# Kernel tuning notes

Hardware: AMD Instinct MI355X
Metric: run time of the kernel (lower is better)

## Reference

```python
import jax, jax.numpy as jnp
import numpy as np

N, E, B = 40000, 640000, 8192
IN, META, HID, OUT = 768, 6, 256, 128
NE, K, REL, NET = 4, 2, 200, 3
NL, NH, FF = 4, 4, 512


def setup_inputs():
    key = jax.random.key(0)
    keys = iter(jax.random.split(key, 64))
    def p(*shape):
        return jax.random.normal(next(keys), shape, jnp.float32) * 0.02
    return dict(
        x=jax.random.normal(next(keys), (N, IN + META), jnp.float32),
        noise=jax.random.normal(next(keys), (3, B, NE), jnp.float32),
        g_lin1_w=p(HID, IN + META), g_lin1_b=p(HID),
        conv_W=p(2, HID, HID), conv_Wr=p(2, HID, REL), conv_a=p(2, 3 * HID),
        conv_Wres=p(2, HID, HID), conv_rel=p(2, NET, REL),
        g_lin2_w=p(OUT, HID), g_lin2_b=p(OUT),
        te_w=p(OUT, IN), te_b=p(OUT),
        me_w1=p(HID, META), me_b1=p(HID), me_w2=p(OUT, HID), me_b2=p(OUT),
        moe_gate_w=p(3, NE, OUT), moe_noise_w=p(3, OUT),
        moe_w1=p(3, NE, 4 * OUT, OUT), moe_b1=p(3, NE, 4 * OUT),
        moe_w2=p(3, NE, OUT, 4 * OUT), moe_b2=p(3, NE, OUT),
        tf_qkv_w=p(NL, 3 * OUT, OUT), tf_qkv_b=p(NL, 3 * OUT),
        tf_out_w=p(NL, OUT, OUT), tf_out_b=p(NL, OUT),
        tf_ln1_g=jnp.ones((NL, OUT), jnp.float32), tf_ln1_b=jnp.zeros((NL, OUT), jnp.float32),
        tf_ff1_w=p(NL, FF, OUT), tf_ff1_b=p(NL, FF),
        tf_ff2_w=p(NL, OUT, FF), tf_ff2_b=p(NL, OUT),
        tf_ln2_g=jnp.ones((NL, OUT), jnp.float32), tf_ln2_b=jnp.zeros((NL, OUT), jnp.float32),
        clf_w=p(2, 3 * OUT), clf_b=p(2),
        edge_index=jax.random.randint(next(keys), (2, E), 0, N),
        edge_type=jax.random.randint(next(keys), (E,), 0, NET),
        batch_size=B,
    )


def _seg_softmax(logit, seg, n):
    m = jax.ops.segment_max(logit, seg, num_segments=n)
    e = jnp.exp(logit - m[seg])
    s = jax.ops.segment_sum(e, seg, num_segments=n)
    return e / (s[seg] + 1e-16)


def _hgn_layer(h, src, dst, et, W, Wr, a, Wres, rel, final):
    n, d = h.shape[0], W.shape[0]
    Wx = h @ W.T  # [N, HID]
    # a(cat(Wx_i, Wx_j, Wr_rel)) decomposed: per-node + per-edge-type scalars
    s_i = Wx @ a[:d]
    s_j = Wx @ a[d:2 * d]
    r_s = (rel @ Wr.T) @ a[2 * d:]  # [NET]
    logit = jax.nn.leaky_relu(s_i[dst] + s_j[src] + r_s[et], 0.2)
    alpha = _seg_softmax(logit, dst, n)
    agg = jax.ops.segment_sum(Wx[src] * alpha[:, None], dst, num_segments=n)
    out = jax.nn.elu(agg + h @ Wres.T)
    if final:
        out = out / jnp.maximum(jnp.linalg.norm(out, axis=1, keepdims=True), 1e-12)
    return out


def _moe(xv, eps, gate_w, noise_w, w1, b1, w2, b2):
    g = xv @ gate_w.T                       # [B, NE]
    nsd = jax.nn.softplus(xv @ noise_w)     # [B]
    h = g + eps * nsd[:, None]
    _, bot = jax.lax.top_k(-h, K)           # bottom-K experts get -inf
    drop = jnp.sum(jax.nn.one_hot(bot, NE, dtype=h.dtype), axis=1) > 0
    h = jnp.where(drop, -jnp.inf, h)
    L = jax.nn.softmax(h, axis=1)
    logits, idx = jax.lax.top_k(L, K)
    tmp = L.sum(0)
    loss = (jnp.std(tmp, ddof=1) / jnp.mean(tmp)) ** 2
    comb = jnp.einsum('bs,bse->be', logits, jax.nn.one_hot(idx, NE, dtype=L.dtype))
    h1 = jax.nn.relu(jnp.einsum('bd,ehd->ebh', xv, w1) + b1[:, None, :])
    eo = jnp.einsum('ebh,eoh->ebo', h1, w2) + b2[:, None, :]  # [NE, B, OUT]
    return jnp.einsum('be,ebo->bo', comb, eo), loss


def _ln(x, g, b):
    mu = x.mean(-1, keepdims=True)
    var = x.var(-1, keepdims=True)
    return (x - mu) / jnp.sqrt(var + 1e-5) * g + b


def _tf_layer(x, qkv_w, qkv_b, out_w, out_b, ln1g, ln1b, f1w, f1b, f2w, f2b, ln2g, ln2b):
    Bq, S, D = x.shape
    hd = D // NH
    qkv = x @ qkv_w.T + qkv_b
    q, k, v = jnp.split(qkv, 3, axis=-1)
    q = q.reshape(Bq, S, NH, hd)
    k = k.reshape(Bq, S, NH, hd)
    v = v.reshape(Bq, S, NH, hd)
    att = jax.nn.softmax(jnp.einsum('bshd,bthd->bhst', q, k) / jnp.sqrt(jnp.float32(hd)), axis=-1)
    o = jnp.einsum('bhst,bthd->bshd', att, v).reshape(Bq, S, D)
    x = _ln(x + o @ out_w.T + out_b, ln1g, ln1b)
    ff = jax.nn.relu(x @ f1w.T + f1b) @ f2w.T + f2b
    return _ln(x + ff, ln2g, ln2b)


def _forward(x, noise, g_lin1_w, g_lin1_b, conv_W, conv_Wr, conv_a, conv_Wres, conv_rel,
             g_lin2_w, g_lin2_b, te_w, te_b, me_w1, me_b1, me_w2, me_b2,
             moe_gate_w, moe_noise_w, moe_w1, moe_b1, moe_w2, moe_b2,
             tf_qkv_w, tf_qkv_b, tf_out_w, tf_out_b, tf_ln1_g, tf_ln1_b,
             tf_ff1_w, tf_ff1_b, tf_ff2_w, tf_ff2_b, tf_ln2_g, tf_ln2_b,
             clf_w, clf_b, edge_index, edge_type, batch_size):
    src, dst = edge_index[0], edge_index[1]
    # graph encoder (dropout is eval no-op)
    h = jax.nn.relu(x @ g_lin1_w.T + g_lin1_b)
    h = _hgn_layer(h, src, dst, edge_type, conv_W[0], conv_Wr[0], conv_a[0], conv_Wres[0], conv_rel[0], False)
    h = _hgn_layer(h, src, dst, edge_type, conv_W[1], conv_Wr[1], conv_a[1], conv_Wres[1], conv_rel[1], True)
    graph = jax.nn.relu(h @ g_lin2_w.T + g_lin2_b)
    x_g = graph[:batch_size]
    text = x[:batch_size, :IN]
    meta = x[:batch_size, IN:]
    x_t = jax.nn.relu(text @ te_w.T + te_b)
    x_m = jax.nn.relu(jax.nn.relu(meta @ me_w1.T + me_b1) @ me_w2.T + me_b2)
    outs, losses = [], []
    for i, xv in enumerate((x_g, x_t, x_m)):
        o, l = _moe(xv, noise[i], moe_gate_w[i], moe_noise_w[i], moe_w1[i], moe_b1[i], moe_w2[i], moe_b2[i])
        outs.append(o)
        losses.append(l)
    loss = losses[0] + losses[1] + losses[2]
    z = jnp.stack(outs, axis=1)  # [B, 3, OUT]
    for li in range(NL):
        z = _tf_layer(z, tf_qkv_w[li], tf_qkv_b[li], tf_out_w[li], tf_out_b[li],
                      tf_ln1_g[li], tf_ln1_b[li], tf_ff1_w[li], tf_ff1_b[li],
                      tf_ff2_w[li], tf_ff2_b[li], tf_ln2_g[li], tf_ln2_b[li])
    logits = z.reshape(z.shape[0], -1) @ clf_w.T + clf_b
    return logits, loss


def reference(x, noise, g_lin1_w, g_lin1_b, conv_W, conv_Wr, conv_a, conv_Wres, conv_rel,
              g_lin2_w, g_lin2_b, te_w, te_b, me_w1, me_b1, me_w2, me_b2,
              moe_gate_w, moe_noise_w, moe_w1, moe_b1, moe_w2, moe_b2,
              tf_qkv_w, tf_qkv_b, tf_out_w, tf_out_b, tf_ln1_g, tf_ln1_b,
              tf_ff1_w, tf_ff1_b, tf_ff2_w, tf_ff2_b, tf_ln2_g, tf_ln2_b,
              clf_w, clf_b, edge_index, edge_type, batch_size):
    return _forward(x, noise, g_lin1_w, g_lin1_b, conv_W, conv_Wr, conv_a, conv_Wres, conv_rel,
                    g_lin2_w, g_lin2_b, te_w, te_b, me_w1, me_b1, me_w2, me_b2,
                    moe_gate_w, moe_noise_w, moe_w1, moe_b1, moe_w2, moe_b2,
                    tf_qkv_w, tf_qkv_b, tf_out_w, tf_out_b, tf_ln1_g, tf_ln1_b,
                    tf_ff1_w, tf_ff1_b, tf_ff2_w, tf_ff2_b, tf_ln2_g, tf_ln2_b,
                    clf_w, clf_b, edge_index, edge_type, batch_size)
```

## Files before the change

### kernel.cpp

```cpp
#include <hip/hip_runtime.h>
#include <hip/hip_bf16.h>
#include <math.h>

#define NN 40000
#define EE 640000
#define BB 8192
#define IN_DIM 768
#define META_DIM 6
#define XDIM 774
#define HID 256
#define OUT_D 128
#define NEXP 4
#define NET_T 3
#define REL_D 200
#define NLAY 4
#define FF_D 512

typedef __attribute__((ext_vector_type(8))) short short8;
typedef __attribute__((ext_vector_type(4))) float f32x4;

__device__ __forceinline__ ushort f2bf(float f) {
    union { float f; unsigned u; } a; a.f = f;
    unsigned u = a.u;
    unsigned r = (u + 0x7FFFu + ((u >> 16) & 1u)) >> 16;
    return (ushort)r;
}
__device__ __forceinline__ float bf2f(ushort h) {
    union { unsigned u; float f; } a; a.u = ((unsigned)h) << 16;
    return a.f;
}
__device__ __forceinline__ unsigned packsplit(float v) {
    ushort h = f2bf(v);
    ushort lo = f2bf(v - bf2f(h));
    return ((unsigned)h << 16) | lo;
}

__global__ void cvt_pack_kernel(const float* __restrict__ src, int ldsrc, int Kreal,
                                unsigned* __restrict__ pk, int R, int ldp)
{
    size_t i = (size_t)blockIdx.x * blockDim.x + threadIdx.x;
    size_t total = (size_t)R * ldp;
    if (i >= total) return;
    int col = (int)(i % ldp);
    int row = (int)(i / ldp);
    float v = (col < Kreal) ? src[(size_t)row * ldsrc + col] : 0.f;
    pk[i] = packsplit(v);
}

static void cvt_pack(const float* src, int ldsrc, int Kreal, unsigned* pk,
                     int R, int ldp, hipStream_t s)
{
    size_t total = (size_t)R * ldp;
    cvt_pack_kernel<<<(int)((total + 255) / 256), 256, 0, s>>>(src, ldsrc, Kreal, pk, R, ldp);
}

template<int ACT, int HAS_RES, int OUT_SPLIT, int A_FP32, int B_PACKED>
__global__ __launch_bounds__(256) void mfma3_128(
    const void* __restrict__ Ap, int lda, int Kreal,
    const void* __restrict__ Bp, int ldb,
    const float* __restrict__ bias, const float* __restrict__ res,
    float* __restrict__ C, unsigned* __restrict__ Cpk,
    int M, int Nn, int K)
{
    __shared__ __align__(16) ushort Ash[128 * 40];
    __shared__ __align__(16) ushort Asl[128 * 40];
    __shared__ __align__(16) ushort Bsh[128 * 40];
    __shared__ __align__(16) ushort Bsl[128 * 40];

    const unsigned* Ak = (const unsigned*)Ap;
    const float*    Af = (const float*)Ap;
    const unsigned* Bk = (const unsigned*)Bp;
    const float*    Bf = (const float*)Bp;

    int bn = blockIdx.x * 128;
    int bm = blockIdx.y * 128;
    int t = threadIdx.x;
    int wave = t >> 6, lane = t & 63;
    int wm = wave & 1, wn = wave >> 1;
    int quad = lane >> 4, r = lane & 15;

    uint4 apk[2][2];
    float afp[2][8];
    uint4 bpk[2][2];
    float bfp[2][8];

    auto loadA = [&](int k0) {
#pragma unroll
        for (int i = 0; i < 2; i++) {
            int idx = t + i * 256;
            int row = idx >> 2, c8 = idx & 3;
            int grow = bm + row; if (grow > M - 1) grow = M - 1;
            if (A_FP32) {
                int cb = k0 + c8 * 8;
                const float* p = Af + (size_t)grow * lda + cb;
                if (cb + 8 <= Kreal) {
                    float2 f0 = *(const float2*)p,       f1 = *(const float2*)(p + 2);
                    float2 f2 = *(const float2*)(p + 4), f3 = *(const float2*)(p + 6);
                    afp[i][0] = f0.x; afp[i][1] = f0.y; afp[i][2] = f1.x; afp[i][3] = f1.y;
                    afp[i][4] = f2.x; afp[i][5] = f2.y; afp[i][6] = f3.x; afp[i][7] = f3.y;
                } else {
#pragma unroll
                    for (int e = 0; e < 8; e++)
                        afp[i][e] = (cb + e < Kreal) ? p[e] : 0.f;
                }
            } else {
                const unsigned* p = Ak + (size_t)grow * lda + k0 + c8 * 8;
                apk[i][0] = *(const uint4*)p; apk[i][1] = *(const uint4*)(p + 4);
            }
        }
    };
    auto loadB = [&](int k0) {
#pragma unroll
        for (int i = 0; i < 2; i++) {
            int idx = t + i * 256;
            int row = idx >> 2, c8 = idx & 3;
            if (B_PACKED) {
                const unsigned* p = Bk + (size_t)(bn + row) * ldb + k0 + c8 * 8;
                bpk[i][0] = *(const uint4*)p; bpk[i][1] = *(const uint4*)(p + 4);
            } else {
                const float* p = Bf + (size_t)(bn + row) * ldb + k0 + c8 * 8;
                float2 f0 = *(const float2*)p,       f1 = *(const float2*)(p + 2);
                float2 f2 = *(const float2*)(p + 4), f3 = *(const float2*)(p + 6);
                bfp[i][0] = f0.x; bfp[i][1] = f0.y; bfp[i][2] = f1.x; bfp[i][3] = f1.y;
                bfp[i][4] = f2.x; bfp[i][5] = f2.y; bfp[i][6] = f3.x; bfp[i][7] = f3.y;
            }
        }
    };
    auto storeTiles = [&]() {
#pragma unroll
        for (int i = 0; i < 2; i++) {
            int idx = t + i * 256;
            int row = idx >> 2, c8 = idx & 3;
            short8 hi, lo;
            if (A_FP32) {
#pragma unroll
                for (int e = 0; e < 8; e++) {
                    ushort h = f2bf(afp[i][e]);
                    hi[e] = (short)h;
                    lo[e] = (short)f2bf(afp[i][e] - bf2f(h));
                }
            } else {
                unsigned u[8] = {apk[i][0].x, apk[i][0].y, apk[i][0].z, apk[i][0].w,
                                 apk[i][1].x, apk[i][1].y, apk[i][1].z, apk[i][1].w};
#pragma unroll
                for (int e = 0; e < 8; e++) { hi[e] = (short)(u[e] >> 16); lo[e] = (short)(u[e] & 0xFFFFu); }
            }
            *(short8*)&Ash[row * 40 + c8 * 8] = hi;
            *(short8*)&Asl[row * 40 + c8 * 8] = lo;
        }
#pragma unroll
        for (int i = 0; i < 2; i++) {
            int idx = t + i * 256;
            int row = idx >> 2, c8 = idx & 3;
            short8 hi, lo;
            if (B_PACKED) {
                unsigned u[8] = {bpk[i][0].x, bpk[i][0].y, bpk[i][0].z, bpk[i][0].w,
                                 bpk[i][1].x, bpk[i][1].y, bpk[i][1].z, bpk[i][1].w};
#pragma unroll
                for (int e = 0; e < 8; e++) { hi[e] = (short)(u[e] >> 16); lo[e] = (short)(u[e] & 0xFFFFu); }
            } else {
#pragma unroll
                for (int e = 0; e < 8; e++) {
                    ushort h = f2bf(bfp[i][e]);
                    hi[e] = (short)h;
                    lo[e] = (short)f2bf(bfp[i][e] - bf2f(h));
                }
            }
            *(short8*)&Bsh[row * 40 + c8 * 8] = hi;
            *(short8*)&Bsl[row * 40 + c8 * 8] = lo;
        }
    };

    f32x4 acc[4][4];
#pragma unroll
    for (int i = 0; i < 4; i++)
#pragma unroll
        for (int j = 0; j < 4; j++) acc[i][j] = (f32x4){0.f, 0.f, 0.f, 0.f};

    loadA(0); loadB(0);
    for (int k0 = 0; k0 < K; k0 += 32) {
        storeTiles();
        __syncthreads();
        if (k0 + 32 < K) { loadA(k0 + 32); loadB(k0 + 32); }

        short8 ah[4], al[4];
#pragma unroll
        for (int i = 0; i < 4; i++) {
            int ro = (wm * 64 + i * 16 + r) * 40 + quad * 8;
            ah[i] = *(const short8*)&Ash[ro];
            al[i] = *(const short8*)&Asl[ro];
        }
#pragma unroll
        for (int j = 0; j < 4; j++) {
            int ro = (wn * 64 + j * 16 + r) * 40 + quad * 8;
            short8 bh = *(const short8*)&Bsh[ro];
            short8 bl = *(const short8*)&Bsl[ro];
#pragma unroll
            for (int i = 0; i < 4; i++)
                acc[i][j] = __builtin_amdgcn_mfma_f32_16x16x32_bf16(ah[i], bh, acc[i][j], 0, 0, 0);
#pragma unroll
            for (int i = 0; i < 4; i++)
                acc[i][j] = __builtin_amdgcn_mfma_f32_16x16x32_bf16(ah[i], bl, acc[i][j], 0, 0, 0);
#pragma unroll
            for (int i = 0; i < 4; i++)
                acc[i][j] = __builtin_amdgcn_mfma_f32_16x16x32_bf16(al[i], bh, acc[i][j], 0, 0, 0);
        }
        __syncthreads();
    }

#pragma unroll
    for (int j = 0; j < 4; j++) {
        int col = bn + wn * 64 + j * 16 + r;
        float bc = bias ? bias[col] : 0.f;
#pragma unroll
        for (int i = 0; i < 4; i++) {
#pragma unroll
            for (int reg = 0; reg < 4; reg++) {
                int row = bm + wm * 64 + i * 16 + quad * 4 + reg;
                if (row >= M) continue;
                float v = acc[i][j][reg] + bc;
                if (HAS_RES) v += res[(size_t)row * Nn + col];
                if (ACT == 1) v = fmaxf(v, 0.f);
                else if (ACT == 2) v = (v > 0.f) ? v : expm1f(v);
                if (OUT_SPLIT) Cpk[(size_t)row * Nn + col] = packsplit(v);
                else           C[(size_t)row * Nn + col] = v;
            }
        }
    }
}

template<int ACT, int HAS_RES, int OUT_SPLIT, int A_FP32, int B_PACKED>
static void m128_launch(const void* Ap, int lda, int Kreal, const void* Bp, int ldb,
                        const float* bias, const float* res,
                        float* C, unsigned* Cpk,
                        int M, int Nn, int K, hipStream_t s)
{
    dim3 grid(Nn / 128, (M + 127) / 128);
    mfma3_128<ACT, HAS_RES, OUT_SPLIT, A_FP32, B_PACKED><<<grid, 256, 0, s>>>(
        Ap, lda, Kreal, Bp, ldb, bias, res, C, Cpk, M, Nn, K);
}

template<int WM, int ACT, int HAS_RES, int OUT_SPLIT, int A_FP32, int B_PACKED>
__global__ __launch_bounds__(256) void mfma3k(
    const void* __restrict__ Ap, int lda, int Kreal,
    const void* __restrict__ Bp, int ldb,
    const float* __restrict__ bias, const float* __restrict__ res,
    float* __restrict__ C, unsigned* __restrict__ Cpk,
    int M, int Nn, int K)
{
    const int BM = 32 * WM;
    __shared__ __align__(16) ushort Ash[BM * 40];
    __shared__ __align__(16) ushort Asl[BM * 40];
    __shared__ __align__(16) ushort Bsh[64 * 40];
    __shared__ __align__(16) ushort Bsl[64 * 40];

    const unsigned* Ak = (const unsigned*)Ap;
    const float*    Af = (const float*)Ap;
    const unsigned* Bk = (const unsigned*)Bp;
    const float*    Bf = (const float*)Bp;

    int bn = blockIdx.x * 64;
    int bm = blockIdx.y * BM;
    int t = threadIdx.x;
    int wave = t >> 6, lane = t & 63;
    int wm = wave & 1, wn = wave >> 1;
    int quad = lane >> 4, r = lane & 15;

    const int ACH = (BM * 4) / 256;

    uint4 apk[2][2];
    float afp[2][8];
    uint4 bpk[2];
    float4 bfp[2];

    auto loadA = [&](int k0) {
#pragma unroll
        for (int i = 0; i < ACH; i++) {
            int idx = t + i * 256;
            int row = idx >> 2, c8 = idx & 3;
            int grow = bm + row; if (grow > M - 1) grow = M - 1;
            if (A_FP32) {
                int cb = k0 + c8 * 8;
                const float* p = Af + (size_t)grow * lda + cb;
                if (cb + 8 <= Kreal) {
                    float2 f0 = *(const float2*)p,       f1 = *(const float2*)(p + 2);
                    float2 f2 = *(const float2*)(p + 4), f3 = *(const float2*)(p + 6);
                    afp[i][0] = f0.x; afp[i][1] = f0.y; afp[i][2] = f1.x; afp[i][3] = f1.y;
                    afp[i][4] = f2.x; afp[i][5] = f2.y; afp[i][6] = f3.x; afp[i][7] = f3.y;
                } else {
#pragma unroll
                    for (int e = 0; e < 8; e++)
                        afp[i][e] = (cb + e < Kreal) ? p[e] : 0.f;
                }
            } else {
                const unsigned* p = Ak + (size_t)grow * lda + k0 + c8 * 8;
                apk[i][0] = *(const uint4*)p; apk[i][1] = *(const uint4*)(p + 4);
            }
        }
    };
    auto loadB = [&](int k0) {
        int row = t >> 2, c8 = t & 3;
        if (B_PACKED) {
            const unsigned* p = Bk + (size_t)(bn + row) * ldb + k0 + c8 * 8;
            bpk[0] = *(const uint4*)p; bpk[1] = *(const uint4*)(p + 4);
        } else {
            const float* p = Bf + (size_t)(bn + row) * ldb + k0 + c8 * 8;
            bfp[0] = *(const float4*)p; bfp[1] = *(const float4*)(p + 4);
        }
    };
    auto storeTiles = [&]() {
#pragma unroll
        for (int i = 0; i < ACH; i++) {
            int idx = t + i * 256;
            int row = idx >> 2, c8 = idx & 3;
            short8 hi, lo;
            if (A_FP32) {
#pragma unroll
                for (int e = 0; e < 8; e++) {
                    ushort h = f2bf(afp[i][e]);
                    hi[e] = (short)h;
                    lo[e] = (short)f2bf(afp[i][e] - bf2f(h));
                }
            } else {
                unsigned u[8] = {apk[i][0].x, apk[i][0].y, apk[i][0].z, apk[i][0].w,
                                 apk[i][1].x, apk[i][1].y, apk[i][1].z, apk[i][1].w};
#pragma unroll
                for (int e = 0; e < 8; e++) { hi[e] = (short)(u[e] >> 16); lo[e] = (short)(u[e] & 0xFFFFu); }
            }
            *(short8*)&Ash[row * 40 + c8 * 8] = hi;
            *(short8*)&Asl[row * 40 + c8 * 8] = lo;
        }
        {
            int row = t >> 2, c8 = t & 3;
            short8 hi, lo;
            if (B_PACKED) {
                unsigned u[8] = {bpk[0].x, bpk[0].y, bpk[0].z, bpk[0].w,
                                 bpk[1].x, bpk[1].y, bpk[1].z, bpk[1].w};
#pragma unroll
                for (int e = 0; e < 8; e++) { hi[e] = (short)(u[e] >> 16); lo[e] = (short)(u[e] & 0xFFFFu); }
            } else {
                float f[8] = {bfp[0].x, bfp[0].y, bfp[0].z, bfp[0].w,
                              bfp[1].x, bfp[1].y, bfp[1].z, bfp[1].w};
#pragma unroll
                for (int e = 0; e < 8; e++) {
                    ushort h = f2bf(f[e]);
                    hi[e] = (short)h;
                    lo[e] = (short)f2bf(f[e] - bf2f(h));
                }
            }
            *(short8*)&Bsh[row * 40 + c8 * 8] = hi;
            *(short8*)&Bsl[row * 40 + c8 * 8] = lo;
        }
    };

    f32x4 acc[WM][2];
#pragma unroll
    for (int i = 0; i < WM; i++)
#pragma unroll
        for (int j = 0; j < 2; j++) acc[i][j] = (f32x4){0.f, 0.f, 0.f, 0.f};

    loadA(0); loadB(0);
    for (int k0 = 0; k0 < K; k0 += 32) {
        storeTiles();
        __syncthreads();
        if (k0 + 32 < K) { loadA(k0 + 32); loadB(k0 + 32); }

        short8 ah[WM], al[WM];
#pragma unroll
        for (int i = 0; i < WM; i++) {
            int ro = (wm * (WM * 16) + i * 16 + r) * 40 + quad * 8;
            ah[i] = *(const short8*)&Ash[ro];
            al[i] = *(const short8*)&Asl[ro];
        }
#pragma unroll
        for (int j = 0; j < 2; j++) {
            int ro = (wn * 32 + j * 16 + r) * 40 + quad * 8;
            short8 bh = *(const short8*)&Bsh[ro];
            short8 bl = *(const short8*)&Bsl[ro];
#pragma unroll
            for (int i = 0; i < WM; i++)
                acc[i][j] = __builtin_amdgcn_mfma_f32_16x16x32_bf16(ah[i], bh, acc[i][j], 0, 0, 0);
#pragma unroll
            for (int i = 0; i < WM; i++)
                acc[i][j] = __builtin_amdgcn_mfma_f32_16x16x32_bf16(ah[i], bl, acc[i][j], 0, 0, 0);
#pragma unroll
            for (int i = 0; i < WM; i++)
                acc[i][j] = __builtin_amdgcn_mfma_f32_16x16x32_bf16(al[i], bh, acc[i][j], 0, 0, 0);
        }
        __syncthreads();
    }

#pragma unroll
    for (int j = 0; j < 2; j++) {
        int col = bn + wn * 32 + j * 16 + r;
        float bc = bias ? bias[col] : 0.f;
#pragma unroll
        for (int i = 0; i < WM; i++) {
#pragma unroll
            for (int reg = 0; reg < 4; reg++) {
                int row = bm + wm * (WM * 16) + i * 16 + quad * 4 + reg;
                if (row >= M) continue;
                float v = acc[i][j][reg] + bc;
                if (HAS_RES) v += res[(size_t)row * Nn + col];
                if (ACT == 1) v = fmaxf(v, 0.f);
                else if (ACT == 2) v = (v > 0.f) ? v : expm1f(v);
                if (OUT_SPLIT) Cpk[(size_t)row * Nn + col] = packsplit(v);
                else           C[(size_t)row * Nn + col] = v;
            }
        }
    }
}

template<int WM, int ACT, int HAS_RES, int OUT_SPLIT, int A_FP32, int B_PACKED>
static void m3_launch(const void* Ap, int lda, int Kreal, const void* Bp, int ldb,
                      const float* bias, const float* res,
                      float* C, unsigned* Cpk,
                      int M, int Nn, int K, hipStream_t s)
{
    const int BM = 32 * WM;
    dim3 grid(Nn / 64, (M + BM - 1) / BM);
    mfma3k<WM, ACT, HAS_RES, OUT_SPLIT, A_FP32, B_PACKED><<<grid, 256, 0, s>>>(
        Ap, lda, Kreal, Bp, ldb, bias, res, C, Cpk, M, Nn, K);
}

template<int ACT>
__global__ void gemm_kernel(const float* __restrict__ A, int lda,
                            const float* __restrict__ Bw,
                            const float* __restrict__ bias,
                            const float* __restrict__ res,
                            float* __restrict__ C, int M, int Nn, int K)
{
    __shared__ float As[16][68];
    __shared__ float Bs[16][68];
    int bm = blockIdx.y * 64, bn = blockIdx.x * 64;
    int t = threadIdx.x;
    int tx = t & 15, ty = t >> 4;
    float acc[4][4] = {{0.f}};

    for (int k0 = 0; k0 < K; k0 += 16) {
#pragma unroll
        for (int i = 0; i < 4; i++) {
            int l = t * 4 + i; int mm = l >> 4, kk = l & 15;
            int gm = bm + mm, gk = k0 + kk;
            As[kk][mm] = (gm < M && gk < K) ? A[(size_t)gm * lda + gk] : 0.f;
        }
#pragma unroll
        for (int i = 0; i < 4; i++) {
            int l = t * 4 + i; int nn = l >> 4, kk = l & 15;
            int gn = bn + nn, gk = k0 + kk;
            Bs[kk][nn] = (gn < Nn && gk < K) ? Bw[(size_t)gn * K + gk] : 0.f;
        }
        __syncthreads();
#pragma unroll
        for (int kk = 0; kk < 16; kk++) {
            float4 a4 = *reinterpret_cast<const float4*>(&As[kk][ty * 4]);
            float4 b4 = *reinterpret_cast<const float4*>(&Bs[kk][tx * 4]);
            float a0[4] = {a4.x, a4.y, a4.z, a4.w};
            float b0[4] = {b4.x, b4.y, b4.z, b4.w};
#pragma unroll
            for (int i = 0; i < 4; i++)
#pragma unroll
                for (int j = 0; j < 4; j++)
                    acc[i][j] += a0[i] * b0[j];
        }
        __syncthreads();
    }
#pragma unroll
    for (int i = 0; i < 4; i++) {
        int gm = bm + ty * 4 + i; if (gm >= M) continue;
#pragma unroll
        for (int j = 0; j < 4; j++) {
            int gn = bn + tx * 4 + j; if (gn >= Nn) continue;
            float v = acc[i][j];
            if (bias) v += bias[gn];
            if (res)  v += res[(size_t)gm * Nn + gn];
            if (ACT == 1) v = fmaxf(v, 0.f);
            C[(size_t)gm * Nn + gn] = v;
        }
    }
}

template<int ACT, int A_BF16, int OUT_BF16>
__global__ __launch_bounds__(256) void mfma_gemm(
    const void* __restrict__ Ap, size_t strideAz,
    const float* __restrict__ Bw, size_t strideBz,
    const float* __restrict__ bias, size_t strideBiasz,
    void* __restrict__ Cp, size_t strideCz,
    int M, int Nn, int K)
{
    __shared__ __align__(16) ushort As[64 * 40];
    __shared__ __align__(16) ushort Bs[64 * 40];

    int z = blockIdx.z;
    const float*  Af  = (const float*)Ap  + (A_BF16 ? 0 : z * strideAz);
    const ushort* Ab  = (const ushort*)Ap + (A_BF16 ? z * strideAz : 0);
    const float*  Bwz = Bw + z * strideBz;
    const float*  bz  = bias ? bias + z * strideBiasz : nullptr;
    float*  Cf = (float*)Cp  + (OUT_BF16 ? 0 : z * strideCz);
    ushort* Cb = (ushort*)Cp + (OUT_BF16 ? z * strideCz : 0);

    int bn = blockIdx.x * 64;
    int bm = blockIdx.y * 64;
    int t = threadIdx.x;
    int wave = t >> 6, lane = t & 63;
    int wm = wave & 1, wn = wave >> 1;
    int quad = lane >> 4, r = lane & 15;

    short8 apre_b;
    float4 apre_f[2];
    float4 bpre[2];
    int ar = t >> 2, ac = t & 3;

    auto loadA = [&](int k0) {
        if (A_BF16) {
            apre_b = *(const short8*)(Ab + (size_t)(bm + ar) * K + k0 + ac * 8);
        } else {
#pragma unroll
            for (int i = 0; i < 2; i++) {
                int idx = t + i * 256;
                int row = idx >> 3, c4 = idx & 7;
                apre_f[i] = *(const float4*)(Af + (size_t)(bm + row) * K + k0 + c4 * 4);
            }
        }
    };
    auto loadB = [&](int k0) {
        const float* p = Bwz + (size_t)(bn + ar) * K + k0 + ac * 8;
        bpre[0] = *(const float4*)p;
        bpre[1] = *(const float4*)(p + 4);
    };
    auto storeTiles = [&]() {
        if (A_BF16) {
            *(short8*)&As[ar * 40 + ac * 8] = apre_b;
        } else {
#pragma unroll
            for (int i = 0; i < 2; i++) {
                int idx = t + i * 256;
                int row = idx >> 3, c4 = idx & 7;
                ushort4 u;
                u.x = f2bf(apre_f[i].x); u.y = f2bf(apre_f[i].y);
                u.z = f2bf(apre_f[i].z); u.w = f2bf(apre_f[i].w);
                *(ushort4*)&As[row * 40 + c4 * 4] = u;
            }
        }
        {
            float f[8] = {bpre[0].x, bpre[0].y, bpre[0].z, bpre[0].w,
                          bpre[1].x, bpre[1].y, bpre[1].z, bpre[1].w};
            short8 hb;
#pragma unroll
            for (int e = 0; e < 8; e++) hb[e] = (short)f2bf(f[e]);
            *(short8*)&Bs[ar * 40 + ac * 8] = hb;
        }
    };

    f32x4 acc[2][2];
#pragma unroll
    for (int i = 0; i < 2; i++)
#pragma unroll
        for (int j = 0; j < 2; j++) acc[i][j] = (f32x4){0.f, 0.f, 0.f, 0.f};

    loadA(0); loadB(0);
    for (int k0 = 0; k0 < K; k0 += 32) {
        storeTiles();
        __syncthreads();
        if (k0 + 32 < K) { loadA(k0 + 32); loadB(k0 + 32); }

        short8 af[2];
#pragma unroll
        for (int i = 0; i < 2; i++)
            af[i] = *(const short8*)&As[(wm * 32 + i * 16 + r) * 40 + quad * 8];
#pragma unroll
        for (int j = 0; j < 2; j++) {
            short8 bf = *(const short8*)&Bs[(wn * 32 + j * 16 + r) * 40 + quad * 8];
#pragma unroll
            for (int i = 0; i < 2; i++)
                acc[i][j] = __builtin_amdgcn_mfma_f32_16x16x32_bf16(af[i], bf, acc[i][j], 0, 0, 0);
        }
        __syncthreads();
    }

#pragma unroll
    for (int j = 0; j < 2; j++) {
        int col = bn + wn * 32 + j * 16 + r;
        float bc = bz ? bz[col] : 0.f;
#pragma unroll
        for (int i = 0; i < 2; i++) {
#pragma unroll
            for (int reg = 0; reg < 4; reg++) {
                int row = bm + wm * 32 + i * 16 + quad * 4 + reg;
                float v = acc[i][j][reg] + bc;
                if (ACT == 1) v = fmaxf(v, 0.f);
                if (OUT_BF16) Cb[(size_t)row * Nn + col] = f2bf(v);
                else          Cf[(size_t)row * Nn + col] = v;
            }
        }
    }
}

template<int ACT, int A_BF16, int OUT_BF16>
static void mfma_launch(const void* A, size_t sAz, const float* Bw, size_t sBz,
                        const float* bias, size_t sbz, void* C, size_t sCz,
                        int M, int Nn, int K, int batch, hipStream_t s)
{
    dim3 grid(Nn / 64, M / 64, batch);
    mfma_gemm<ACT, A_BF16, OUT_BF16><<<grid, 256, 0, s>>>(A, sAz, Bw, sBz, bias, sbz, C, sCz, M, Nn, K);
}

__global__ void sisj_kernel(const float* __restrict__ Wx, const float* __restrict__ a,
                            float* __restrict__ s_i, float* __restrict__ s_j, int n)
{
    int t = threadIdx.x; int w = t >> 6, l = t & 63;
    int m = blockIdx.x * 4 + w; if (m >= n) return;
    const float* r = Wx + (size_t)m * HID;
    float v1 = 0.f, v2 = 0.f;
#pragma unroll
    for (int i = 0; i < 4; i++) {
        float xv = r[l + 64 * i];
        v1 += xv * a[l + 64 * i];
        v2 += xv * a[HID + l + 64 * i];
    }
    for (int off = 32; off; off >>= 1) { v1 += __shfl_down(v1, off); v2 += __shfl_down(v2, off); }
    if (l == 0) { s_i[m] = v1; s_j[m] = v2; }
}

__global__ void rs_kernel(const float* __restrict__ Wr, const float* __restrict__ rel,
                          const float* __restrict__ a3, float* __restrict__ rs)
{
    __shared__ float red[256];
    int tt = blockIdx.x; int j = threadIdx.x;
    const float* relr = rel + tt * REL_D;
    const float* wr = Wr + (size_t)j * REL_D;
    float wsum = 0.f;
    for (int k = 0; k < REL_D; k++) wsum += wr[k] * relr[k];
    red[j] = wsum * a3[j];
    __syncthreads();
    for (int s2 = 128; s2; s2 >>= 1) { if (j < s2) red[j] += red[j + s2]; __syncthreads(); }
    if (j == 0) rs[tt] = red[0];
}

__global__ void deg_kernel(const int* __restrict__ dst, int* __restrict__ deg)
{
    int e = blockIdx.x * blockDim.x + threadIdx.x;
    if (e < EE) atomicAdd(&deg[dst[e]], 1);
}

__global__ void scan_kernel(const int* __restrict__ deg, int* __restrict__ rowstart,
                            int* __restrict__ cursor, int n)
{
    __shared__ int bs[1024];
    int t = threadIdx.x;
    int base = t * 40;
    int loc[40];
    int sum = 0;
#pragma unroll
    for (int i = 0; i < 40; i++) {
        int v = (base + i < n) ? deg[base + i] : 0;
        loc[i] = sum; sum += v;
    }
    bs[t] = sum;
    __syncthreads();
    for (int off = 1; off < 1024; off <<= 1) {
        int x = (t >= off) ? bs[t - off] : 0;
        __syncthreads();
        bs[t] += x;
        __syncthreads();
    }
    int excl = bs[t] - sum;
#pragma unroll
    for (int i = 0; i < 40; i++) {
        if (base + i < n) { int v = excl + loc[i]; rowstart[base + i] = v; cursor[base + i] = v; }
    }
    if (t == 1023) rowstart[n] = bs[1023];
}

__global__ void fill_kernel(const int* __restrict__ src, const int* __restrict__ dst,
                            const int* __restrict__ et, int* __restrict__ cursor,
                            unsigned* __restrict__ csr_val)
{
    int e = blockIdx.x * blockDim.x + threadIdx.x;
    if (e >= EE) return;
    int d = dst[e];
    int pos = atomicAdd(&cursor[d], 1);
    csr_val[pos] = (unsigned)src[e] | ((unsigned)et[e] << 16);
}

__global__ void csr_agg_kernel(const unsigned* __restrict__ csr_val,
                               const int* __restrict__ rowstart,
                               const float* __restrict__ s_i, const float* __restrict__ s_j,
                               const float* __restrict__ rsv,
                               const float* __restrict__ Wx, float* __restrict__ agg,
                               int nlim)
{
    int t = threadIdx.x; int w = t >> 6, l = t & 63;
    int node = blockIdx.x * 4 + w; if (node >= nlim) return;
    int start = rowstart[node], end = rowstart[node + 1];
    float r0 = rsv[0], r1 = rsv[1], r2 = rsv[2];
    float si = s_i[node];

    float m = -INFINITY;
    for (int i = start + l; i < end; i += 64) {
        unsigned v = csr_val[i];
        int s = v & 0xFFFF; int et = v >> 16;
        float rr = (et == 0) ? r0 : ((et == 1) ? r1 : r2);
        float lg = si + s_j[s] + rr;
        lg = (lg >= 0.f) ? lg : 0.2f * lg;
        m = fmaxf(m, lg);
    }
    for (int off = 32; off; off >>= 1) m = fmaxf(m, __shfl_down(m, off));
    m = __shfl(m, 0);

    float a0 = 0.f, a1 = 0.f, a2 = 0.f, a3 = 0.f, ssum = 0.f;
    for (int c = start; c < end; c += 64) {
        int nchunk = min(64, end - c);
        float wgt = 0.f; int sidx = 0;
        if (l < nchunk) {
            unsigned v = csr_val[c + l];
            sidx = v & 0xFFFF; int et = v >> 16;
            float rr = (et == 0) ? r0 : ((et == 1) ? r1 : r2);
            float lg = si + s_j[sidx] + rr;
            lg = (lg >= 0.f) ? lg : 0.2f * lg;
            wgt = expf(lg - m);
            ssum += wgt;
        }
        int j = 0;
        for (; j + 4 <= nchunk; j += 4) {
            float w0 = __shfl(wgt, j),     w1 = __shfl(wgt, j + 1);
            float w2 = __shfl(wgt, j + 2), w3 = __shfl(wgt, j + 3);
            int s0 = __shfl(sidx, j),     s1 = __shfl(sidx, j + 1);
            int s2 = __shfl(sidx, j + 2), s3 = __shfl(sidx, j + 3);
            const float* p0 = Wx + (size_t)s0 * HID + l;
            const float* p1 = Wx + (size_t)s1 * HID + l;
            const float* p2 = Wx + (size_t)s2 * HID + l;
            const float* p3 = Wx + (size_t)s3 * HID + l;
            float v00 = p0[0], v01 = p0[64], v02 = p0[128], v03 = p0[192];
            float v10 = p1[0], v11 = p1[64], v12 = p1[128], v13 = p1[192];
            float v20 = p2[0], v21 = p2[64], v22 = p2[128], v23 = p2[192];
            float v30 = p3[0], v31 = p3[64], v32 = p3[128], v33 = p3[192];
            a0 += w0 * v00 + w1 * v10 + w2 * v20 + w3 * v30;
            a1 += w0 * v01 + w1 * v11 + w2 * v21 + w3 * v31;
            a2 += w0 * v02 + w1 * v12 + w2 * v22 + w3 * v32;
            a3 += w0 * v03 + w1 * v13 + w2 * v23 + w3 * v33;
        }
        for (; j < nchunk; j++) {
            float wj = __shfl(wgt, j);
            int sj = __shfl(sidx, j);
            const float* wr = Wx + (size_t)sj * HID + l;
            a0 += wj * wr[0];
            a1 += wj * wr[64];
            a2 += wj * wr[128];
            a3 += wj * wr[192];
        }
    }
    for (int off = 32; off; off >>= 1) ssum += __shfl_down(ssum, off);
    ssum = __shfl(ssum, 0);
    float inv = 1.f / (ssum + 1e-16f);
    float* ar = agg + (size_t)node * HID;
    ar[l] = a0 * inv; ar[l + 64] = a1 * inv; ar[l + 128] = a2 * inv; ar[l + 192] = a3 * inv;
}

__global__ void rownorm_pack(unsigned* __restrict__ pk, int n)
{
    int t = threadIdx.x; int w = t >> 6, l = t & 63;
    int m = blockIdx.x * 4 + w; if (m >= n) return;
    size_t base = (size_t)m * HID;
    float vals[4]; float q = 0.f;
#pragma unroll
    for (int i = 0; i < 4; i++) {
        unsigned u = pk[base + l + 64 * i];
        vals[i] = bf2f((ushort)(u >> 16)) + bf2f((ushort)(u & 0xFFFFu));
        q += vals[i] * vals[i];
    }
    for (int off = 32; off; off >>= 1) q += __shfl_down(q, off);
    q = __shfl(q, 0);
    float inv = 1.f / fmaxf(sqrtf(q), 1e-12f);
#pragma unroll
    for (int i = 0; i < 4; i++)
        pk[base + l + 64 * i] = packsplit(vals[i] * inv);
}

__global__ void moe_gate_kernel(const float* __restrict__ xv, const float* __restrict__ gate_w,
                                const float* __restrict__ noise_w, const float* __restrict__ eps,
                                float* __restrict__ comb, float* __restrict__ tmpsum)
{
    __shared__ float part[4];
    int t = threadIdx.x; int w = t >> 6, l = t & 63;
    if (t < 4) part[t] = 0.f;
    __syncthreads();
    int b = blockIdx.x * 4 + w;
    const float* xr = xv + (size_t)b * OUT_D;
    float x0 = xr[l], x1 = xr[l + 64];
    float dots[5];
#pragma unroll
    for (int e = 0; e < 4; e++) {
        const float* gw = gate_w + e * OUT_D;
        float v = x0 * gw[l] + x1 * gw[l + 64];
        for (int off = 32; off; off >>= 1) v += __shfl_down(v, off);
        dots[e] = v;
    }
    {
        float v = x0 * noise_w[l] + x1 * noise_w[l + 64];
        for (int off = 32; off; off >>= 1) v += __shfl_down(v, off);
        dots[4] = v;
    }
    if (l == 0) {
        float xg = dots[4];
        float nsd = (xg > 20.f) ? xg : log1pf(expf(xg));
        float hv[4];
#pragma unroll
        for (int e = 0; e < 4; e++) hv[e] = dots[e] + eps[(size_t)b * 4 + e] * nsd;
        int i1 = 0;
        for (int e = 1; e < 4; e++) if (hv[e] < hv[i1]) i1 = e;
        int i2 = -1;
        for (int e = 0; e < 4; e++) { if (e == i1) continue; if (i2 < 0 || hv[e] < hv[i2]) i2 = e; }
        int k1 = -1, k2 = -1;
        for (int e = 0; e < 4; e++) { if (e != i1 && e != i2) { if (k1 < 0) k1 = e; else k2 = e; } }
        float mm = fmaxf(hv[k1], hv[k2]);
        float e1 = expf(hv[k1] - mm), e2 = expf(hv[k2] - mm);
        float s = e1 + e2;
        float L[4] = {0.f, 0.f, 0.f, 0.f};
        L[k1] = e1 / s; L[k2] = e2 / s;
#pragma unroll
        for (int e = 0; e < 4; e++) comb[(size_t)b * 4 + e] = L[e];
        atomicAdd(&part[k1], L[k1]);
        atomicAdd(&part[k2], L[k2]);
    }
    __syncthreads();
    if (t < 4) atomicAdd(&tmpsum[t], part[t]);
}

__global__ void moe_combine_kernel(const float* __restrict__ eo, const float* __restrict__ comb,
                                   float* __restrict__ zout)
{
    int idx = blockIdx.x * blockDim.x + threadIdx.x;
    if (idx >= BB * OUT_D) return;
    int b = idx >> 7, o = idx & 127;
    const size_t S = (size_t)BB * OUT_D;
    float v = comb[b * 4 + 0] * eo[idx] + comb[b * 4 + 1] * eo[idx + S]
            + comb[b * 4 + 2] * eo[idx + 2 * S] + comb[b * 4 + 3] * eo[idx + 3 * S];
    zout[(size_t)b * (3 * OUT_D) + o] = v;
}

__global__ void loss_kernel(const float* __restrict__ tmpsum, float* __restrict__ out)
{
    if (threadIdx.x == 0 && blockIdx.x == 0) {
        float total = 0.f;
        for (int v = 0; v < 3; v++) {
            const float* tp = tmpsum + v * 4;
            float mean = (tp[0] + tp[1] + tp[2] + tp[3]) * 0.25f;
            float var = 0.f;
            for (int e = 0; e < 4; e++) { float d = tp[e] - mean; var += d * d; }
            var /= 3.f;
            float r = sqrtf(var) / mean;
            total += r * r;
        }
        out[0] = total;
    }
}

__global__ void attn_kernel(const float* __restrict__ qkv, float* __restrict__ o)
{
    int t = threadIdx.x;
    int half = t >> 5;
    int d = t & 31;
    int task = blockIdx.x * 8 + half;
    int b = task >> 2, h = task & 3;
    const float* base = qkv + (size_t)b * 3 * 384 + h * 32;
    float q0 = base[d],       q1 = base[384 + d],       q2 = base[768 + d];
    float k0 = base[128 + d], k1 = base[384 + 128 + d], k2 = base[768 + 128 + d];
    float v0 = base[256 + d], v1 = base[384 + 256 + d], v2 = base[768 + 256 + d];
    float s[3][3];
    s[0][0] = q0 * k0; s[0][1] = q0 * k1; s[0][2] = q0 * k2;
    s[1][0] = q1 * k0; s[1][1] = q1 * k1; s[1][2] = q1 * k2;
    s[2][0] = q2 * k0; s[2][1] = q2 * k1; s[2][2] = q2 * k2;
#pragma unroll
    for (int i = 0; i < 3; i++)
#pragma unroll
        for (int j = 0; j < 3; j++) {
            float v = s[i][j];
            for (int off = 16; off; off >>= 1) v += __shfl_xor(v, off, 32);
            s[i][j] = v;
        }
    const float scale = 0.17677669529663687f;
    float outv[3];
#pragma unroll
    for (int i = 0; i < 3; i++) {
        float a0 = s[i][0] * scale, a1 = s[i][1] * scale, a2 = s[i][2] * scale;
        float m = fmaxf(a0, fmaxf(a1, a2));
        float e0 = expf(a0 - m), e1 = expf(a1 - m), e2 = expf(a2 - m);
        float inv = 1.f / (e0 + e1 + e2);
        outv[i] = (e0 * v0 + e1 * v1 + e2 * v2) * inv;
    }
    float* ob = o + (size_t)b * 3 * 128 + h * 32;
    ob[d] = outv[0]; ob[128 + d] = outv[1]; ob[256 + d] = outv[2];
}

__global__ void ln_residual_kernel(float* __restrict__ x, const float* __restrict__ add,
                                   const float* __restrict__ g, const float* __restrict__ bta, int M)
{
    int t = threadIdx.x; int w = t >> 6, l = t & 63;
    int row = blockIdx.x * 4 + w; if (row >= M) return;
    float* xr = x + (size_t)row * 128;
    const float* ar = add + (size_t)row * 128;
    float v0 = xr[l] + ar[l], v1 = xr[l + 64] + ar[l + 64];
    float s = v0 + v1;
    for (int off = 32; off; off >>= 1) s += __shfl_down(s, off);
    s = __shfl(s, 0);
    float mu = s * (1.f / 128.f);
    float d0 = v0 - mu, d1 = v1 - mu;
    float q = d0 * d0 + d1 * d1;
    for (int off = 32; off; off >>= 1) q += __shfl_down(q, off);
    q = __shfl(q, 0);
    float inv = rsqrtf(q * (1.f / 128.f) + 1e-5f);
    xr[l]      = d0 * inv * g[l] + bta[l];
    xr[l + 64] = d1 * inv * g[l + 64] + bta[l + 64];
}

__global__ void clf_kernel(const float* __restrict__ z, const float* __restrict__ w,
                           const float* __restrict__ b, float* __restrict__ out)
{
    int t = threadIdx.x; int wv = t >> 6, l = t & 63;
    int row = blockIdx.x * 4 + wv; if (row >= BB) return;
    const float* zr = z + (size_t)row * 384;
    float v0 = 0.f, v1 = 0.f;
    for (int i = l; i < 384; i += 64) {
        float zz = zr[i];
        v0 += zz * w[i];
        v1 += zz * w[384 + i];
    }
    for (int off = 32; off; off >>= 1) { v0 += __shfl_down(v0, off); v1 += __shfl_down(v1, off); }
    if (l == 0) { out[row * 2] = v0 + b[0]; out[row * 2 + 1] = v1 + b[1]; }
}

extern "C" void kernel_launch(void* const* d_in, const int* in_sizes, int n_in,
                              void* d_out, int out_size, void* d_ws, size_t ws_size,
                              hipStream_t stream)
{
    const float* x         = (const float*)d_in[0];
    const float* noise     = (const float*)d_in[1];
    const float* g_lin1_w  = (const float*)d_in[2];
    const float* g_lin1_b  = (const float*)d_in[3];
    const float* conv_W    = (const float*)d_in[4];
    const float* conv_Wr   = (const float*)d_in[5];
    const float* conv_a    = (const float*)d_in[6];
    const float* conv_Wres = (const float*)d_in[7];
    const float* conv_rel  = (const float*)d_in[8];
    const float* g_lin2_w  = (const float*)d_in[9];
    const float* g_lin2_b  = (const float*)d_in[10];
    const float* te_w      = (const float*)d_in[11];
    const float* te_b      = (const float*)d_in[12];
    const float* me_w1     = (const float*)d_in[13];
    const float* me_b1     = (const float*)d_in[14];
    const float* me_w2     = (const float*)d_in[15];
    const float* me_b2     = (const float*)d_in[16];
    const float* moe_gate_w  = (const float*)d_in[17];
    const float* moe_noise_w = (const float*)d_in[18];
    const float* moe_w1    = (const float*)d_in[19];
    const float* moe_b1    = (const float*)d_in[20];
    const float* moe_w2    = (const float*)d_in[21];
    const float* moe_b2    = (const float*)d_in[22];
    const float* tf_qkv_w  = (const float*)d_in[23];
    const float* tf_qkv_b  = (const float*)d_in[24];
    const float* tf_out_w  = (const float*)d_in[25];
    const float* tf_out_b  = (const float*)d_in[26];
    const float* tf_ln1_g  = (const float*)d_in[27];
    const float* tf_ln1_b  = (const float*)d_in[28];
    const float* tf_ff1_w  = (const float*)d_in[29];
    const float* tf_ff1_b  = (const float*)d_in[30];
    const float* tf_ff2_w  = (const float*)d_in[31];
    const float* tf_ff2_b  = (const float*)d_in[32];
    const float* tf_ln2_g  = (const float*)d_in[33];
    const float* tf_ln2_b  = (const float*)d_in[34];
    const float* clf_w     = (const float*)d_in[35];
    const float* clf_b     = (const float*)d_in[36];
    const int*   edge_index = (const int*)d_in[37];
    const int*   edge_type  = (const int*)d_in[38];

    float* ws = (float*)d_ws;

    const size_t F_A = 0;
    const size_t F_B = 10240000;
    const size_t F_C = 22822912;
    const size_t F_D = 33062912;
    const size_t F_M = 43302912;
    const size_t F_X = 44200000;

    unsigned* hApk = (unsigned*)(ws + F_A);
    float* qkv    = ws + F_A;
    float* wx     = ws + F_B;
    float* graph  = ws + F_B;
    ushort* ff1bf = (ushort*)(ws + F_B);
    float* agg    = ws + F_C;
    float* x_mh   = ws + F_C;
    ushort* h1bf  = (ushort*)(ws + F_C);
    float* attn_o = ws + F_C;
    float* tmp1   = ws + F_C + 3200000;
    unsigned* hBpk = (unsigned*)(ws + F_D);
    float* z      = ws + F_D;
    float* x_t    = ws + F_D + 3200000;
    float* x_m    = ws + F_D + 4300000;
    float* eo     = ws + F_D + 5400000;

    float* s_i    = ws + F_M;
    float* s_j    = ws + F_M + 40000;
    float* rsv    = ws + F_M + 80000;
    float* comb   = ws + F_M + 80016;
    float* tmpsum = ws + F_M + 112784;
    int* deg      = (int*)(ws + F_M + 120000);
    int* rowstart = (int*)(ws + F_M + 161000);
    int* cursor   = (int*)(ws + F_M + 202000);
    unsigned* csr_val = (unsigned*)(ws + F_M + 242000);

    unsigned* wpk  = (unsigned*)(ws + F_X);

    const int* srcv = edge_index;
    const int* dstv = edge_index + EE;

    hipMemsetAsync(deg, 0, NN * sizeof(int), stream);
    deg_kernel<<<(EE + 255) / 256, 256, 0, stream>>>(dstv, deg);
    scan_kernel<<<1, 1024, 0, stream>>>(deg, rowstart, cursor, NN);
    fill_kernel<<<(EE + 255) / 256, 256, 0, stream>>>(srcv, dstv, edge_type, cursor, csr_val);

    cvt_pack(g_lin1_w, XDIM, XDIM, wpk, HID, 800, stream);
    m128_launch<1, 0, 1, 1, 1>(x, XDIM, XDIM, wpk, 800, g_lin1_b, nullptr,
                               nullptr, hApk, NN, HID, 800, stream);

    unsigned *inpk = hApk, *outpk = hBpk;
    for (int layer = 0; layer < 2; layer++) {
        const float* W    = conv_W    + (size_t)layer * HID * HID;
        const float* Wr   = conv_Wr   + (size_t)layer * HID * REL_D;
        const float* a    = conv_a    + (size_t)layer * 3 * HID;
        const float* Wres = conv_Wres + (size_t)layer * HID * HID;
        const float* rel  = conv_rel  + (size_t)layer * NET_T * REL_D;
        int mOut = (layer == 1) ? BB : NN;

        m128_launch<0, 0, 0, 0, 0>(inpk, HID, HID, W, HID, nullptr, nullptr,
                                   wx, nullptr, NN, HID, HID, stream);
        sisj_kernel<<<NN / 4, 256, 0, stream>>>(wx, a, s_i, s_j, NN);
        rs_kernel<<<NET_T, 256, 0, stream>>>(Wr, rel, a + 2 * HID, rsv);
        csr_agg_kernel<<<(mOut + 3) / 4, 256, 0, stream>>>(csr_val, rowstart, s_i, s_j, rsv, wx, agg, mOut);
        if (layer == 0)
            m128_launch<2, 1, 1, 0, 0>(inpk, HID, HID, Wres, HID, nullptr, agg,
                                       nullptr, outpk, mOut, HID, HID, stream);
        else
            m3_launch<2, 2, 1, 1, 0, 0>(inpk, HID, HID, Wres, HID, nullptr, agg,
                                        nullptr, outpk, mOut, HID, HID, stream);
        unsigned* tp = inpk; inpk = outpk; outpk = tp;
    }
    rownorm_pack<<<BB / 4, 256, 0, stream>>>(inpk, BB);

    m3_launch<2, 1, 0, 0, 0, 0>(inpk, HID, HID, g_lin2_w, HID, g_lin2_b, nullptr,
                                graph, nullptr, BB, OUT_D, HID, stream);

    m3_launch<2, 1, 0, 0, 1, 0>(x, XDIM, IN_DIM, te_w, IN_DIM, te_b, nullptr,
                                x_t, nullptr, BB, OUT_D, IN_DIM, stream);
    {
        dim3 g((HID + 63) / 64, (BB + 63) / 64);
        gemm_kernel<1><<<g, 256, 0, stream>>>(x + IN_DIM, XDIM, me_w1, me_b1, nullptr,
                                              x_mh, BB, HID, META_DIM);
    }
    m3_launch<2, 1, 0, 0, 1, 0>(x_mh, HID, HID, me_w2, HID, me_b2, nullptr,
                                x_m, nullptr, BB, OUT_D, HID, stream);

    hipMemsetAsync(tmpsum, 0, 16 * sizeof(float), stream);
    const float* xvs[3] = { graph, x_t, x_m };
    for (int v = 0; v < 3; v++) {
        const float* xv = xvs[v];
        moe_gate_kernel<<<BB / 4, 256, 0, stream>>>(
            xv, moe_gate_w + (size_t)v * NEXP * OUT_D, moe_noise_w + (size_t)v * OUT_D,
            noise + (size_t)v * BB * NEXP, comb, tmpsum + v * 4);
        mfma_launch<1, 0, 1>(xv, 0,
                             moe_w1 + (size_t)v * 4 * FF_D * OUT_D, (size_t)FF_D * OUT_D,
                             moe_b1 + (size_t)v * 4 * FF_D, FF_D,
                             h1bf, (size_t)BB * FF_D,
                             BB, FF_D, OUT_D, 4, stream);
        mfma_launch<0, 1, 0>(h1bf, (size_t)BB * FF_D,
                             moe_w2 + (size_t)v * 4 * OUT_D * FF_D, (size_t)OUT_D * FF_D,
                             moe_b2 + (size_t)v * 4 * OUT_D, OUT_D,
                             eo, (size_t)BB * OUT_D,
                             BB, OUT_D, FF_D, 4, stream);
        moe_combine_kernel<<<(BB * OUT_D) / 256, 256, 0, stream>>>(eo, comb, z + v * OUT_D);
    }

    const int MT = BB * 3;
    for (int li = 0; li < NLAY; li++) {
        mfma_launch<0, 0, 0>(z, 0, tf_qkv_w + (size_t)li * 384 * 128, 0,
                             tf_qkv_b + li * 384, 0, qkv, 0, MT, 384, 128, 1, stream);
        attn_kernel<<<(BB * 4) / 8, 256, 0, stream>>>(qkv, attn_o);
        mfma_launch<0, 0, 0>(attn_o, 0, tf_out_w + (size_t)li * 128 * 128, 0,
                             tf_out_b + li * 128, 0, tmp1, 0, MT, 128, 128, 1, stream);
        ln_residual_kernel<<<MT / 4, 256, 0, stream>>>(z, tmp1, tf_ln1_g + li * 128, tf_ln1_b + li * 128, MT);
        mfma_launch<1, 0, 1>(z, 0, tf_ff1_w + (size_t)li * 512 * 128, 0,
                             tf_ff1_b + li * 512, 0, ff1bf, 0, MT, 512, 128, 1, stream);
        mfma_launch<0, 1, 0>(ff1bf, 0, tf_ff2_w + (size_t)li * 128 * 512, 0,
                             tf_ff2_b + li * 128, 0, tmp1, 0, MT, 128, 512, 1, stream);
        ln_residual_kernel<<<MT / 4, 256, 0, stream>>>(z, tmp1, tf_ln2_g + li * 128, tf_ln2_b + li * 128, MT);
    }

    clf_kernel<<<BB / 4, 256, 0, stream>>>(z, clf_w, clf_b, (float*)d_out);
    loss_kernel<<<1, 64, 0, stream>>>(tmpsum, (float*)d_out + BB * 2);
}
```

Before: 1.551 ms.

## Pre-pack input features into split-bf16 once and reuse across GEMMs

Adds a conversion pass that packs the full fp32 feature matrix into a padded split-bf16 (hi/lo) buffer. The first graph linear layer and the text-embedding GEMM then read this packed buffer instead of converting fp32 on the fly inside each tile load. The A_FP32 path is removed from the 128-tile kernel, and the remaining fp32 loads are widened from float2 to float4. The cost is an extra full pass over x plus a large workspace region, and the bandwidth saved by avoiding repeated in-kernel conversion may not pay for that pass.

```diff
diff --git a/kernel.cpp b/kernel.cpp
--- a/kernel.cpp
+++ b/kernel.cpp
@@ -54,9 +54,9 @@
     cvt_pack_kernel<<<(int)((total + 255) / 256), 256, 0, s>>>(src, ldsrc, Kreal, pk, R, ldp);
 }
 
-template<int ACT, int HAS_RES, int OUT_SPLIT, int A_FP32, int B_PACKED>
+template<int ACT, int HAS_RES, int OUT_SPLIT, int B_PACKED>
 __global__ __launch_bounds__(256) void mfma3_128(
-    const void* __restrict__ Ap, int lda, int Kreal,
+    const unsigned* __restrict__ Ak, int lda,
     const void* __restrict__ Bp, int ldb,
     const float* __restrict__ bias, const float* __restrict__ res,
     float* __restrict__ C, unsigned* __restrict__ Cpk,
@@ -67,8 +67,6 @@
     __shared__ __align__(16) ushort Bsh[128 * 40];
     __shared__ __align__(16) ushort Bsl[128 * 40];
 
-    const unsigned* Ak = (const unsigned*)Ap;
-    const float*    Af = (const float*)Ap;
     const unsigned* Bk = (const unsigned*)Bp;
     const float*    Bf = (const float*)Bp;
 
@@ -80,9 +78,8 @@
     int quad = lane >> 4, r = lane & 15;
 
     uint4 apk[2][2];
-    float afp[2][8];
     uint4 bpk[2][2];
-    float bfp[2][8];
+    float4 bfp[2][2];
 
     auto loadA = [&](int k0) {
 #pragma unroll
@@ -90,23 +87,8 @@
             int idx = t + i * 256;
             int row = idx >> 2, c8 = idx & 3;
             int grow = bm + row; if (grow > M - 1) grow = M - 1;
-            if (A_FP32) {
-                int cb = k0 + c8 * 8;
-                const float* p = Af + (size_t)grow * lda + cb;
-                if (cb + 8 <= Kreal) {
-                    float2 f0 = *(const float2*)p,       f1 = *(const float2*)(p + 2);
-                    float2 f2 = *(const float2*)(p + 4), f3 = *(const float2*)(p + 6);
-                    afp[i][0] = f0.x; afp[i][1] = f0.y; afp[i][2] = f1.x; afp[i][3] = f1.y;
-                    afp[i][4] = f2.x; afp[i][5] = f2.y; afp[i][6] = f3.x; afp[i][7] = f3.y;
-                } else {
-#pragma unroll
-                    for (int e = 0; e < 8; e++)
-                        afp[i][e] = (cb + e < Kreal) ? p[e] : 0.f;
-                }
-            } else {
-                const unsigned* p = Ak + (size_t)grow * lda + k0 + c8 * 8;
-                apk[i][0] = *(const uint4*)p; apk[i][1] = *(const uint4*)(p + 4);
-            }
+            const unsigned* p = Ak + (size_t)grow * lda + k0 + c8 * 8;
+            apk[i][0] = *(const uint4*)p; apk[i][1] = *(const uint4*)(p + 4);
         }
     };
     auto loadB = [&](int k0) {
@@ -119,10 +101,7 @@
                 bpk[i][0] = *(const uint4*)p; bpk[i][1] = *(const uint4*)(p + 4);
             } else {
                 const float* p = Bf + (size_t)(bn + row) * ldb + k0 + c8 * 8;
-                float2 f0 = *(const float2*)p,       f1 = *(const float2*)(p + 2);
-                float2 f2 = *(const float2*)(p + 4), f3 = *(const float2*)(p + 6);
-                bfp[i][0] = f0.x; bfp[i][1] = f0.y; bfp[i][2] = f1.x; bfp[i][3] = f1.y;
-                bfp[i][4] = f2.x; bfp[i][5] = f2.y; bfp[i][6] = f3.x; bfp[i][7] = f3.y;
+                bfp[i][0] = *(const float4*)p; bfp[i][1] = *(const float4*)(p + 4);
             }
         }
     };
@@ -131,20 +110,11 @@
         for (int i = 0; i < 2; i++) {
             int idx = t + i * 256;
             int row = idx >> 2, c8 = idx & 3;
+            unsigned u[8] = {apk[i][0].x, apk[i][0].y, apk[i][0].z, apk[i][0].w,
+                             apk[i][1].x, apk[i][1].y, apk[i][1].z, apk[i][1].w};
             short8 hi, lo;
-            if (A_FP32) {
-#pragma unroll
-                for (int e = 0; e < 8; e++) {
-                    ushort h = f2bf(afp[i][e]);
-                    hi[e] = (short)h;
-                    lo[e] = (short)f2bf(afp[i][e] - bf2f(h));
-                }
-            } else {
-                unsigned u[8] = {apk[i][0].x, apk[i][0].y, apk[i][0].z, apk[i][0].w,
-                                 apk[i][1].x, apk[i][1].y, apk[i][1].z, apk[i][1].w};
-#pragma unroll
-                for (int e = 0; e < 8; e++) { hi[e] = (short)(u[e] >> 16); lo[e] = (short)(u[e] & 0xFFFFu); }
-            }
+#pragma unroll
+            for (int e = 0; e < 8; e++) { hi[e] = (short)(u[e] >> 16); lo[e] = (short)(u[e] & 0xFFFFu); }
             *(short8*)&Ash[row * 40 + c8 * 8] = hi;
             *(short8*)&Asl[row * 40 + c8 * 8] = lo;
         }
@@ -159,11 +129,13 @@
 #pragma unroll
                 for (int e = 0; e < 8; e++) { hi[e] = (short)(u[e] >> 16); lo[e] = (short)(u[e] & 0xFFFFu); }
             } else {
+                float f[8] = {bfp[i][0].x, bfp[i][0].y, bfp[i][0].z, bfp[i][0].w,
+                              bfp[i][1].x, bfp[i][1].y, bfp[i][1].z, bfp[i][1].w};
 #pragma unroll
                 for (int e = 0; e < 8; e++) {
-                    ushort h = f2bf(bfp[i][e]);
+                    ushort h = f2bf(f[e]);
                     hi[e] = (short)h;
-                    lo[e] = (short)f2bf(bfp[i][e] - bf2f(h));
+                    lo[e] = (short)f2bf(f[e] - bf2f(h));
                 }
             }
             *(short8*)&Bsh[row * 40 + c8 * 8] = hi;
@@ -229,15 +201,15 @@
     }
 }
 
-template<int ACT, int HAS_RES, int OUT_SPLIT, int A_FP32, int B_PACKED>
-static void m128_launch(const void* Ap, int lda, int Kreal, const void* Bp, int ldb,
+template<int ACT, int HAS_RES, int OUT_SPLIT, int B_PACKED>
+static void m128_launch(const unsigned* Ak, int lda, const void* Bp, int ldb,
                         const float* bias, const float* res,
                         float* C, unsigned* Cpk,
                         int M, int Nn, int K, hipStream_t s)
 {
     dim3 grid(Nn / 128, (M + 127) / 128);
-    mfma3_128<ACT, HAS_RES, OUT_SPLIT, A_FP32, B_PACKED><<<grid, 256, 0, s>>>(
-        Ap, lda, Kreal, Bp, ldb, bias, res, C, Cpk, M, Nn, K);
+    mfma3_128<ACT, HAS_RES, OUT_SPLIT, B_PACKED><<<grid, 256, 0, s>>>(
+        Ak, lda, Bp, ldb, bias, res, C, Cpk, M, Nn, K);
 }
 
 template<int WM, int ACT, int HAS_RES, int OUT_SPLIT, int A_FP32, int B_PACKED>
@@ -283,10 +255,9 @@
                 int cb = k0 + c8 * 8;
                 const float* p = Af + (size_t)grow * lda + cb;
                 if (cb + 8 <= Kreal) {
-                    float2 f0 = *(const float2*)p,       f1 = *(const float2*)(p + 2);
-                    float2 f2 = *(const float2*)(p + 4), f3 = *(const float2*)(p + 6);
-                    afp[i][0] = f0.x; afp[i][1] = f0.y; afp[i][2] = f1.x; afp[i][3] = f1.y;
-                    afp[i][4] = f2.x; afp[i][5] = f2.y; afp[i][6] = f3.x; afp[i][7] = f3.y;
+                    float4 f0 = *(const float4*)p, f1 = *(const float4*)(p + 4);
+                    afp[i][0] = f0.x; afp[i][1] = f0.y; afp[i][2] = f0.z; afp[i][3] = f0.w;
+                    afp[i][4] = f1.x; afp[i][5] = f1.y; afp[i][6] = f1.z; afp[i][7] = f1.w;
                 } else {
 #pragma unroll
                     for (int e = 0; e < 8; e++)
@@ -1009,7 +980,8 @@
     int* cursor   = (int*)(ws + F_M + 202000);
     unsigned* csr_val = (unsigned*)(ws + F_M + 242000);
 
-    unsigned* wpk  = (unsigned*)(ws + F_X);
+    unsigned* xpk  = (unsigned*)(ws + F_X);
+    unsigned* wpk  = (unsigned*)(ws + F_X + 32000000);
 
     const int* srcv = edge_index;
     const int* dstv = edge_index + EE;
@@ -1019,9 +991,10 @@
     scan_kernel<<<1, 1024, 0, stream>>>(deg, rowstart, cursor, NN);
     fill_kernel<<<(EE + 255) / 256, 256, 0, stream>>>(srcv, dstv, edge_type, cursor, csr_val);
 
+    cvt_pack(x, XDIM, XDIM, xpk, NN, 800, stream);
     cvt_pack(g_lin1_w, XDIM, XDIM, wpk, HID, 800, stream);
-    m128_launch<1, 0, 1, 1, 1>(x, XDIM, XDIM, wpk, 800, g_lin1_b, nullptr,
-                               nullptr, hApk, NN, HID, 800, stream);
+    m128_launch<1, 0, 1, 1>(xpk, 800, wpk, 800, g_lin1_b, nullptr,
+                            nullptr, hApk, NN, HID, 800, stream);
 
     unsigned *inpk = hApk, *outpk = hBpk;
     for (int layer = 0; layer < 2; layer++) {
@@ -1032,14 +1005,14 @@
         const float* rel  = conv_rel  + (size_t)layer * NET_T * REL_D;
         int mOut = (layer == 1) ? BB : NN;
 
-        m128_launch<0, 0, 0, 0, 0>(inpk, HID, HID, W, HID, nullptr, nullptr,
-                                   wx, nullptr, NN, HID, HID, stream);
+        m128_launch<0, 0, 0, 0>(inpk, HID, W, HID, nullptr, nullptr,
+                                wx, nullptr, NN, HID, HID, stream);
         sisj_kernel<<<NN / 4, 256, 0, stream>>>(wx, a, s_i, s_j, NN);
         rs_kernel<<<NET_T, 256, 0, stream>>>(Wr, rel, a + 2 * HID, rsv);
         csr_agg_kernel<<<(mOut + 3) / 4, 256, 0, stream>>>(csr_val, rowstart, s_i, s_j, rsv, wx, agg, mOut);
         if (layer == 0)
-            m128_launch<2, 1, 1, 0, 0>(inpk, HID, HID, Wres, HID, nullptr, agg,
-                                       nullptr, outpk, mOut, HID, HID, stream);
+            m128_launch<2, 1, 1, 0>(inpk, HID, Wres, HID, nullptr, agg,
+                                    nullptr, outpk, mOut, HID, HID, stream);
         else
             m3_launch<2, 2, 1, 1, 0, 0>(inpk, HID, HID, Wres, HID, nullptr, agg,
                                         nullptr, outpk, mOut, HID, HID, stream);
@@ -1050,7 +1023,7 @@
     m3_launch<2, 1, 0, 0, 0, 0>(inpk, HID, HID, g_lin2_w, HID, g_lin2_b, nullptr,
                                 graph, nullptr, BB, OUT_D, HID, stream);
 
-    m3_launch<2, 1, 0, 0, 1, 0>(x, XDIM, IN_DIM, te_w, IN_DIM, te_b, nullptr,
+    m3_launch<2, 1, 0, 0, 0, 0>(xpk, 800, IN_DIM, te_w, IN_DIM, te_b, nullptr,
                                 x_t, nullptr, BB, OUT_D, IN_DIM, stream);
     {
         dim3 g((HID + 63) / 64, (BB + 63) / 64);
```

New measurement: 1.544 ms. Within noise of the previous version (-0.5%).
